# Kernel optimization log

Hardware: AMD Instinct MI355X
Metric: run time of the kernel (lower is better)

Reference implementation:

```python
import jax, jax.numpy as jnp
import numpy as np
from jax import lax

B, H, N, F = 32, 168, 512, 8
P_STEPS = 24


def setup_inputs() -> dict:
    key = jax.random.key(0)
    ks = jax.random.split(key, 8)
    s = 0.02
    return {
        "x": jax.random.normal(ks[0], (B, H, N, F), dtype=jnp.float32),
        "conv_w": jax.random.normal(ks[1], (N * F, N), dtype=jnp.float32) * s,
        "conv_b": jnp.zeros((N,), dtype=jnp.float32),
        "lstm_k": jax.random.normal(ks[2], (N, 4 * N), dtype=jnp.float32) * s,
        "lstm_rk": jax.random.normal(ks[3], (N, 4 * N), dtype=jnp.float32) * s,
        "lstm_b": jnp.zeros((4 * N,), dtype=jnp.float32),
        "dense_w": jax.random.normal(ks[4], (N, N), dtype=jnp.float32) * s,
        "dense_b": jnp.zeros((N,), dtype=jnp.float32),
        "P": P_STEPS,
    }


def _lstm_cell(h, c, x_t, lstm_k, lstm_rk, lstm_b):
    # Keras LSTMCell gate order: i, f, g(candidate), o
    z = x_t @ lstm_k + h @ lstm_rk + lstm_b  # [B, 4N]
    i, f, g, o = jnp.split(z, 4, axis=-1)
    i = jax.nn.sigmoid(i)
    f = jax.nn.sigmoid(f)
    g = jnp.tanh(g)
    o = jax.nn.sigmoid(o)
    c_new = f * c + i * g
    h_new = o * jnp.tanh(c_new)
    return h_new, c_new


def reference(x, conv_w, conv_b, lstm_k, lstm_rk, lstm_b, dense_w, dense_b, P):
    b, hh, n, f = x.shape
    # Conv1D kernel_size=1 == per-timestep dense projection N*F -> N
    xr = x.reshape(b, hh, n * f) @ conv_w + conv_b  # [B, H, N]

    h0 = jnp.zeros((b, n), dtype=x.dtype)
    c0 = jnp.zeros((b, n), dtype=x.dtype)

    def enc_step(carry, x_t):
        h, c = carry
        h, c = _lstm_cell(h, c, x_t, lstm_k, lstm_rk, lstm_b)
        return (h, c), None

    (h, c), _ = lax.scan(enc_step, (h0, c0), xr.transpose(1, 0, 2))

    def dec_step(carry, _):
        h, c = carry
        h2, c2 = _lstm_cell(h, c, h, lstm_k, lstm_rk, lstm_b)
        return (h2, c2), h2

    _, preds = lax.scan(dec_step, (h, c), None, length=P)  # [P, B, N]
    preds = preds.transpose(1, 0, 2)  # [B, P, N]
    return preds @ dense_w + dense_b
```

## Files before the change

### kernel.cpp

```cpp
#include <hip/hip_runtime.h>
#include <hip/hip_bf16.h>
#include <math.h>

typedef __hip_bfloat16 bf16;
typedef __attribute__((ext_vector_type(8))) short short8;
typedef __attribute__((ext_vector_type(4))) float floatx4;

#define B_  32
#define H_  168
#define N_  512
#define P_  24
#define NF_ 4096
#define G4N 2048
#define M1  (B_*H_)
#define NX  (M1*NF_)
#define TSTEPS (H_+P_)
#define NWG 64
#define HSZ (B_*N_)

__global__ __launch_bounds__(256) void cvt_f32_bf16(const float* __restrict__ in,
                                                    bf16* __restrict__ out, int n4) {
  int i = blockIdx.x * 256 + threadIdx.x;
  if (i < n4) {
    float4 v = ((const float4*)in)[i];
    bf16 o[4] = {__float2bfloat16(v.x), __float2bfloat16(v.y),
                 __float2bfloat16(v.z), __float2bfloat16(v.w)};
    *(ulong1*)(out + (size_t)i * 4) = *(ulong1*)o;
  }
}

__global__ __launch_bounds__(256) void transpose_cvt(const float* __restrict__ in,
                                                     bf16* __restrict__ out,
                                                     int R, int C) {
  __shared__ float t[32][33];
  int bx = blockIdx.x, by = blockIdx.y;
  int tx = threadIdx.x, ty = threadIdx.y;
#pragma unroll
  for (int yy = 0; yy < 32; yy += 8)
    t[ty + yy][tx] = in[(size_t)(by * 32 + ty + yy) * C + bx * 32 + tx];
  __syncthreads();
#pragma unroll
  for (int yy = 0; yy < 32; yy += 8)
    out[(size_t)(bx * 32 + ty + yy) * R + by * 32 + tx] =
        __float2bfloat16(t[tx][ty + yy]);
}

__global__ __launch_bounds__(256) void transpose_add_cvt(const float* __restrict__ in1,
                                                         const float* __restrict__ in2,
                                                         bf16* __restrict__ out,
                                                         int R, int C) {
  __shared__ float t[32][33];
  int bx = blockIdx.x, by = blockIdx.y;
  int tx = threadIdx.x, ty = threadIdx.y;
#pragma unroll
  for (int yy = 0; yy < 32; yy += 8) {
    size_t idx = (size_t)(by * 32 + ty + yy) * C + bx * 32 + tx;
    t[ty + yy][tx] = in1[idx] + in2[idx];
  }
  __syncthreads();
#pragma unroll
  for (int yy = 0; yy < 32; yy += 8)
    out[(size_t)(bx * 32 + ty + yy) * R + by * 32 + tx] =
        __float2bfloat16(t[tx][ty + yy]);
}

template <bool OUT_BF16>
__global__ __launch_bounds__(256) void gemm_bt(const bf16* __restrict__ A,
                                               const bf16* __restrict__ BT,
                                               const float* __restrict__ bias,
                                               void* __restrict__ Cout,
                                               int M, int N, int K, int permute) {
  __shared__ short As[128 * 40];
  __shared__ short Bs[128 * 40];
  int tid  = threadIdx.x;
  int wave = tid >> 6, lane = tid & 63;
  int wm = wave >> 1, wn = wave & 1;
  int quad = lane >> 4, l16 = lane & 15;
  int m0 = blockIdx.y * 128, n0 = blockIdx.x * 128;

  floatx4 acc[4][4];
#pragma unroll
  for (int i = 0; i < 4; i++)
#pragma unroll
    for (int j = 0; j < 4; j++) acc[i][j] = (floatx4){0.f, 0.f, 0.f, 0.f};

  int r0 = tid >> 2;
  int c0 = (tid & 3) * 8;

  for (int k0 = 0; k0 < K; k0 += 32) {
    short8 a0 = *(const short8*)(A  + (size_t)(m0 + r0)      * K + k0 + c0);
    short8 a1 = *(const short8*)(A  + (size_t)(m0 + r0 + 64) * K + k0 + c0);
    short8 b0 = *(const short8*)(BT + (size_t)(n0 + r0)      * K + k0 + c0);
    short8 b1 = *(const short8*)(BT + (size_t)(n0 + r0 + 64) * K + k0 + c0);
    __syncthreads();
    *(short8*)(&As[r0 * 40 + c0])        = a0;
    *(short8*)(&As[(r0 + 64) * 40 + c0]) = a1;
    *(short8*)(&Bs[r0 * 40 + c0])        = b0;
    *(short8*)(&Bs[(r0 + 64) * 40 + c0]) = b1;
    __syncthreads();
    short8 af[4], bfr[4];
#pragma unroll
    for (int i = 0; i < 4; i++)
      af[i] = *(const short8*)(&As[(wm * 64 + i * 16 + l16) * 40 + quad * 8]);
#pragma unroll
    for (int j = 0; j < 4; j++)
      bfr[j] = *(const short8*)(&Bs[(wn * 64 + j * 16 + l16) * 40 + quad * 8]);
#pragma unroll
    for (int i = 0; i < 4; i++)
#pragma unroll
      for (int j = 0; j < 4; j++)
        acc[i][j] = __builtin_amdgcn_mfma_f32_16x16x32_bf16(af[i], bfr[j],
                                                            acc[i][j], 0, 0, 0);
  }
#pragma unroll
  for (int i = 0; i < 4; i++) {
    int row = m0 + wm * 64 + i * 16 + quad * 4;
#pragma unroll
    for (int j = 0; j < 4; j++) {
      int col = n0 + wn * 64 + j * 16 + l16;
      float bv = bias ? bias[col] : 0.f;
#pragma unroll
      for (int r = 0; r < 4; r++) {
        int gr = row + r;
        int orow = permute ? (gr % H_) * B_ + gr / H_ : gr;
        float v = acc[i][j][r] + bv;
        if (OUT_BF16)
          ((bf16*)Cout)[(size_t)orow * N + col] = __float2bfloat16(v);
        else
          ((float*)Cout)[(size_t)orow * N + col] = v;
      }
    }
  }
}

__global__ __launch_bounds__(256) void lstm_persist(
    const bf16* __restrict__ rkT,
    const bf16* __restrict__ wcT,
    const float* __restrict__ bvec,
    const float* __restrict__ xk,
    bf16* __restrict__ hring,
    bf16* __restrict__ preds,
    unsigned* __restrict__ bar) {
  __shared__ short Wenc[32][520];
  __shared__ short Wdec[32][520];
  __shared__ float zs[32][33];
  __shared__ bf16  hstage[32][8];

  int tid  = threadIdx.x;
  int wave = tid >> 6, lane = tid & 63;
  int tm = wave >> 1, tn = wave & 1;
  int quad = lane >> 4, l16 = lane & 15;
  int n0 = blockIdx.x * 8;
  int lc   = tn * 16 + l16;
  int gcol = ((lc >> 3) << 9) + n0 + (lc & 7);
  int brow = tm * 16 + quad * 4;

  for (int idx = tid; idx < 32 * 64; idx += 256) {
    int r = idx >> 6, ck = (idx & 63) << 3;
    int grow = ((r >> 3) << 9) + n0 + (r & 7);
    *(short8*)&Wenc[r][ck] = *(const short8*)(rkT + (size_t)grow * 512 + ck);
    *(short8*)&Wdec[r][ck] = *(const short8*)(wcT + (size_t)grow * 512 + ck);
  }
  float bias_r = bvec[gcol];
  int b = tid >> 3, j = tid & 7;
  int nn = n0 + j;
  float c_reg = 0.f;

  float xkv[4];
  {
    const float* xp = xk + (size_t)brow * G4N + gcol;
#pragma unroll
    for (int r = 0; r < 4; ++r) xkv[r] = xp[(size_t)r * G4N];
  }
  __syncthreads();

  for (int t = 0; t < TSTEPS; ++t) {
    const bf16* h_in  = hring + (size_t)t * HSZ;
    bf16*       h_out = hring + (size_t)(t + 1) * HSZ;
    const short(*Ws)[520] = (t < H_) ? Wenc : Wdec;

    float xn[4] = {0.f, 0.f, 0.f, 0.f};
    if (t + 1 < H_) {
      const float* xp = xk + (size_t)((t + 1) * B_ + brow) * G4N + gcol;
#pragma unroll
      for (int r = 0; r < 4; ++r) xn[r] = xp[(size_t)r * G4N];
    }

    floatx4 acc0 = (floatx4){0.f, 0.f, 0.f, 0.f};
    floatx4 acc1 = (floatx4){0.f, 0.f, 0.f, 0.f};
    const bf16*  ap = h_in + (size_t)(tm * 16 + l16) * 512 + quad * 8;
    const short* bp = &Ws[lc][quad * 8];
#pragma unroll
    for (int k0 = 0; k0 < 512; k0 += 64) {
      short8 av0 = *(const short8*)(ap + k0);
      short8 av1 = *(const short8*)(ap + k0 + 32);
      short8 bv0 = *(const short8*)(bp + k0);
      short8 bv1 = *(const short8*)(bp + k0 + 32);
      acc0 = __builtin_amdgcn_mfma_f32_16x16x32_bf16(av0, bv0, acc0, 0, 0, 0);
      acc1 = __builtin_amdgcn_mfma_f32_16x16x32_bf16(av1, bv1, acc1, 0, 0, 0);
    }
    floatx4 acc = acc0 + acc1;
#pragma unroll
    for (int r = 0; r < 4; ++r)
      zs[brow + r][lc] = acc[r] + bias_r + xkv[r];
    __syncthreads();

    float zi = zs[b][j], zf = zs[b][8 + j], zg = zs[b][16 + j], zo = zs[b][24 + j];
    float ig = 1.f / (1.f + __expf(-zi));
    float fg = 1.f / (1.f + __expf(-zf));
    float gg = tanhf(zg);
    float og = 1.f / (1.f + __expf(-zo));
    c_reg = fg * c_reg + ig * gg;
    float hn = og * tanhf(c_reg);
    hstage[b][j] = __float2bfloat16(hn);
    if (t >= H_)
      preds[(size_t)b * (P_ * N_) + (t - H_) * N_ + nn] = __float2bfloat16(hn);
    __syncthreads();

    if (tid < 64) {
      int bb = tid >> 1, f4 = (tid & 1) * 4;
      unsigned long long v = *(const unsigned long long*)&hstage[bb][f4];
      __hip_atomic_store((unsigned long long*)(h_out + bb * 512 + n0 + f4), v,
                         __ATOMIC_RELAXED, __HIP_MEMORY_SCOPE_AGENT);
    }
    __syncthreads();

    if (tid == 0) {
      unsigned old = __hip_atomic_fetch_add(&bar[t], 1u, __ATOMIC_RELAXED,
                                            __HIP_MEMORY_SCOPE_AGENT);
      if (old != NWG - 1) {
        while (__hip_atomic_load(&bar[t], __ATOMIC_RELAXED,
                                 __HIP_MEMORY_SCOPE_AGENT) < NWG)
          __builtin_amdgcn_s_sleep(1);
      }
    }
    __builtin_amdgcn_fence(__ATOMIC_ACQUIRE, "workgroup");
    __syncthreads();
#pragma unroll
    for (int r = 0; r < 4; ++r) xkv[r] = xn[r];
  }
}

extern "C" void kernel_launch(void* const* d_in, const int* in_sizes, int n_in,
                              void* d_out, int out_size, void* d_ws, size_t ws_size,
                              hipStream_t stream) {
  const float* x       = (const float*)d_in[0];
  const float* conv_w  = (const float*)d_in[1];
  const float* conv_b  = (const float*)d_in[2];
  const float* lstm_k  = (const float*)d_in[3];
  const float* lstm_rk = (const float*)d_in[4];
  const float* lstm_b  = (const float*)d_in[5];
  const float* dense_w = (const float*)d_in[6];
  const float* dense_b = (const float*)d_in[7];
  float* out = (float*)d_out;

  char* p = (char*)d_ws;
  auto carve = [&](size_t bytes) {
    char* r = p;
    p += (bytes + 255) & ~(size_t)255;
    return r;
  };
  bf16*  xb    = (bf16*)carve((size_t)NX * 2);
  bf16*  xr    = (bf16*)carve((size_t)M1 * N_ * 2);
  float* xk    = (float*)carve((size_t)M1 * G4N * 4);
  bf16*  cwT   = (bf16*)carve((size_t)N_ * NF_ * 2);
  bf16*  kT    = (bf16*)carve((size_t)G4N * N_ * 2);
  bf16*  rkT   = (bf16*)carve((size_t)G4N * N_ * 2);
  bf16*  wcT   = (bf16*)carve((size_t)G4N * N_ * 2);
  bf16*  dwT   = (bf16*)carve((size_t)N_ * N_ * 2);
  bf16*  preds = (bf16*)carve((size_t)B_ * P_ * N_ * 2);
  bf16*  hring = (bf16*)carve((size_t)(TSTEPS + 1) * HSZ * 2);
  unsigned* bar  = (unsigned*)carve((size_t)TSTEPS * 4);

  cvt_f32_bf16<<<(NX / 4 + 255) / 256, 256, 0, stream>>>(x, xb, NX / 4);
  dim3 tb(32, 8);
  transpose_cvt<<<dim3(N_ / 32, NF_ / 32), tb, 0, stream>>>(conv_w, cwT, NF_, N_);
  transpose_cvt<<<dim3(G4N / 32, N_ / 32), tb, 0, stream>>>(lstm_k, kT, N_, G4N);
  transpose_cvt<<<dim3(G4N / 32, N_ / 32), tb, 0, stream>>>(lstm_rk, rkT, N_, G4N);
  transpose_add_cvt<<<dim3(G4N / 32, N_ / 32), tb, 0, stream>>>(lstm_k, lstm_rk,
                                                                wcT, N_, G4N);
  transpose_cvt<<<dim3(N_ / 32, N_ / 32), tb, 0, stream>>>(dense_w, dwT, N_, N_);
  hipMemsetAsync(hring, 0, (size_t)HSZ * 2, stream);
  hipMemsetAsync(bar, 0, (size_t)TSTEPS * 4, stream);

  gemm_bt<true><<<dim3(N_ / 128, M1 / 128), 256, 0, stream>>>(xb, cwT, conv_b, xr,
                                                              M1, N_, NF_, 1);
  gemm_bt<false><<<dim3(G4N / 128, M1 / 128), 256, 0, stream>>>(xr, kT, nullptr,
                                                                xk, M1, G4N, N_, 0);

  lstm_persist<<<NWG, 256, 0, stream>>>(rkT, wcT, lstm_b, xk, hring, preds, bar);

  gemm_bt<false><<<dim3(N_ / 128, (B_ * P_) / 128), 256, 0, stream>>>(
      preds, dwT, dense_b, out, B_ * P_, N_, N_, 0);
}
```

Measured before the change: 1.038 ms.

## Fuse x bf16 conversion into conv GEMM, merge LSTM weight transposes, skip last barrier

The separate pass that converts the fp32 input to bf16 is removed. The conv GEMM now loads fp32 A tiles directly and converts them in registers, so the full bf16 copy of x is no longer written and read back. The three LSTM weight transpose kernels are merged into one that reads k and rk once and writes kT, rkT and their sum. The grid barrier after the final recurrent step is skipped. The trade-off is that the conv GEMM now reads twice as many A bytes from global memory per tile, and those are fp32 loads, which can raise load latency in the GEMM.

```diff
diff --git a/kernel.cpp b/kernel.cpp
--- a/kernel.cpp
+++ b/kernel.cpp
@@ -18,17 +18,6 @@
 #define NWG 64
 #define HSZ (B_*N_)
 
-__global__ __launch_bounds__(256) void cvt_f32_bf16(const float* __restrict__ in,
-                                                    bf16* __restrict__ out, int n4) {
-  int i = blockIdx.x * 256 + threadIdx.x;
-  if (i < n4) {
-    float4 v = ((const float4*)in)[i];
-    bf16 o[4] = {__float2bfloat16(v.x), __float2bfloat16(v.y),
-                 __float2bfloat16(v.z), __float2bfloat16(v.w)};
-    *(ulong1*)(out + (size_t)i * 4) = *(ulong1*)o;
-  }
-}
-
 __global__ __launch_bounds__(256) void transpose_cvt(const float* __restrict__ in,
                                                      bf16* __restrict__ out,
                                                      int R, int C) {
@@ -45,27 +34,41 @@
         __float2bfloat16(t[tx][ty + yy]);
 }
 
-__global__ __launch_bounds__(256) void transpose_add_cvt(const float* __restrict__ in1,
-                                                         const float* __restrict__ in2,
-                                                         bf16* __restrict__ out,
-                                                         int R, int C) {
-  __shared__ float t[32][33];
+__global__ __launch_bounds__(256) void transpose3_cvt(
+    const float* __restrict__ k_, const float* __restrict__ rk_,
+    bf16* __restrict__ kT, bf16* __restrict__ rkT, bf16* __restrict__ wcT,
+    int R, int C) {
+  __shared__ float t1[32][33];
+  __shared__ float t2[32][33];
   int bx = blockIdx.x, by = blockIdx.y;
   int tx = threadIdx.x, ty = threadIdx.y;
 #pragma unroll
   for (int yy = 0; yy < 32; yy += 8) {
     size_t idx = (size_t)(by * 32 + ty + yy) * C + bx * 32 + tx;
-    t[ty + yy][tx] = in1[idx] + in2[idx];
+    t1[ty + yy][tx] = k_[idx];
+    t2[ty + yy][tx] = rk_[idx];
   }
   __syncthreads();
 #pragma unroll
-  for (int yy = 0; yy < 32; yy += 8)
-    out[(size_t)(bx * 32 + ty + yy) * R + by * 32 + tx] =
-        __float2bfloat16(t[tx][ty + yy]);
-}
-
-template <bool OUT_BF16>
-__global__ __launch_bounds__(256) void gemm_bt(const bf16* __restrict__ A,
+  for (int yy = 0; yy < 32; yy += 8) {
+    size_t o = (size_t)(bx * 32 + ty + yy) * R + by * 32 + tx;
+    float kv = t1[tx][ty + yy], rv = t2[tx][ty + yy];
+    kT[o]  = __float2bfloat16(kv);
+    rkT[o] = __float2bfloat16(rv);
+    wcT[o] = __float2bfloat16(kv + rv);
+  }
+}
+
+__device__ __forceinline__ short8 cvt8(float4 a, float4 b) {
+  bf16 o[8] = {__float2bfloat16(a.x), __float2bfloat16(a.y),
+               __float2bfloat16(a.z), __float2bfloat16(a.w),
+               __float2bfloat16(b.x), __float2bfloat16(b.y),
+               __float2bfloat16(b.z), __float2bfloat16(b.w)};
+  return *(short8*)o;
+}
+
+template <bool A_F32, bool OUT_BF16>
+__global__ __launch_bounds__(256) void gemm_bt(const void* __restrict__ Ain,
                                                const bf16* __restrict__ BT,
                                                const float* __restrict__ bias,
                                                void* __restrict__ Cout,
@@ -88,8 +91,18 @@
   int c0 = (tid & 3) * 8;
 
   for (int k0 = 0; k0 < K; k0 += 32) {
-    short8 a0 = *(const short8*)(A  + (size_t)(m0 + r0)      * K + k0 + c0);
-    short8 a1 = *(const short8*)(A  + (size_t)(m0 + r0 + 64) * K + k0 + c0);
+    short8 a0, a1;
+    if (A_F32) {
+      const float* Af = (const float*)Ain;
+      const float* p0 = Af + (size_t)(m0 + r0)      * K + k0 + c0;
+      const float* p1 = Af + (size_t)(m0 + r0 + 64) * K + k0 + c0;
+      a0 = cvt8(*(const float4*)p0, *(const float4*)(p0 + 4));
+      a1 = cvt8(*(const float4*)p1, *(const float4*)(p1 + 4));
+    } else {
+      const bf16* Ab = (const bf16*)Ain;
+      a0 = *(const short8*)(Ab + (size_t)(m0 + r0)      * K + k0 + c0);
+      a1 = *(const short8*)(Ab + (size_t)(m0 + r0 + 64) * K + k0 + c0);
+    }
     short8 b0 = *(const short8*)(BT + (size_t)(n0 + r0)      * K + k0 + c0);
     short8 b1 = *(const short8*)(BT + (size_t)(n0 + r0 + 64) * K + k0 + c0);
     __syncthreads();
@@ -225,17 +238,19 @@
     }
     __syncthreads();
 
-    if (tid == 0) {
-      unsigned old = __hip_atomic_fetch_add(&bar[t], 1u, __ATOMIC_RELAXED,
-                                            __HIP_MEMORY_SCOPE_AGENT);
-      if (old != NWG - 1) {
-        while (__hip_atomic_load(&bar[t], __ATOMIC_RELAXED,
-                                 __HIP_MEMORY_SCOPE_AGENT) < NWG)
-          __builtin_amdgcn_s_sleep(1);
+    if (t + 1 < TSTEPS) {
+      if (tid == 0) {
+        unsigned old = __hip_atomic_fetch_add(&bar[t], 1u, __ATOMIC_RELAXED,
+                                              __HIP_MEMORY_SCOPE_AGENT);
+        if (old != NWG - 1) {
+          while (__hip_atomic_load(&bar[t], __ATOMIC_RELAXED,
+                                   __HIP_MEMORY_SCOPE_AGENT) < NWG)
+            __builtin_amdgcn_s_sleep(1);
+        }
       }
-    }
-    __builtin_amdgcn_fence(__ATOMIC_ACQUIRE, "workgroup");
-    __syncthreads();
+      __builtin_amdgcn_fence(__ATOMIC_ACQUIRE, "workgroup");
+      __syncthreads();
+    }
 #pragma unroll
     for (int r = 0; r < 4; ++r) xkv[r] = xn[r];
   }
@@ -260,7 +275,6 @@
     p += (bytes + 255) & ~(size_t)255;
     return r;
   };
-  bf16*  xb    = (bf16*)carve((size_t)NX * 2);
   bf16*  xr    = (bf16*)carve((size_t)M1 * N_ * 2);
   float* xk    = (float*)carve((size_t)M1 * G4N * 4);
   bf16*  cwT   = (bf16*)carve((size_t)N_ * NF_ * 2);
@@ -272,24 +286,22 @@
   bf16*  hring = (bf16*)carve((size_t)(TSTEPS + 1) * HSZ * 2);
   unsigned* bar  = (unsigned*)carve((size_t)TSTEPS * 4);
 
-  cvt_f32_bf16<<<(NX / 4 + 255) / 256, 256, 0, stream>>>(x, xb, NX / 4);
   dim3 tb(32, 8);
   transpose_cvt<<<dim3(N_ / 32, NF_ / 32), tb, 0, stream>>>(conv_w, cwT, NF_, N_);
-  transpose_cvt<<<dim3(G4N / 32, N_ / 32), tb, 0, stream>>>(lstm_k, kT, N_, G4N);
-  transpose_cvt<<<dim3(G4N / 32, N_ / 32), tb, 0, stream>>>(lstm_rk, rkT, N_, G4N);
-  transpose_add_cvt<<<dim3(G4N / 32, N_ / 32), tb, 0, stream>>>(lstm_k, lstm_rk,
-                                                                wcT, N_, G4N);
+  transpose3_cvt<<<dim3(G4N / 32, N_ / 32), tb, 0, stream>>>(lstm_k, lstm_rk,
+                                                             kT, rkT, wcT,
+                                                             N_, G4N);
   transpose_cvt<<<dim3(N_ / 32, N_ / 32), tb, 0, stream>>>(dense_w, dwT, N_, N_);
   hipMemsetAsync(hring, 0, (size_t)HSZ * 2, stream);
   hipMemsetAsync(bar, 0, (size_t)TSTEPS * 4, stream);
 
-  gemm_bt<true><<<dim3(N_ / 128, M1 / 128), 256, 0, stream>>>(xb, cwT, conv_b, xr,
-                                                              M1, N_, NF_, 1);
-  gemm_bt<false><<<dim3(G4N / 128, M1 / 128), 256, 0, stream>>>(xr, kT, nullptr,
-                                                                xk, M1, G4N, N_, 0);
+  gemm_bt<true, true><<<dim3(N_ / 128, M1 / 128), 256, 0, stream>>>(
+      x, cwT, conv_b, xr, M1, N_, NF_, 1);
+  gemm_bt<false, false><<<dim3(G4N / 128, M1 / 128), 256, 0, stream>>>(
+      xr, kT, nullptr, xk, M1, G4N, N_, 0);
 
   lstm_persist<<<NWG, 256, 0, stream>>>(rkT, wcT, lstm_b, xk, hring, preds, bar);
 
-  gemm_bt<false><<<dim3(N_ / 128, (B_ * P_) / 128), 256, 0, stream>>>(
+  gemm_bt<false, false><<<dim3(N_ / 128, (B_ * P_) / 128), 256, 0, stream>>>(
       preds, dwT, dense_b, out, B_ * P_, N_, N_, 0);
 }
```

New measurement: 1.069 ms. +3.0%, slower.
